# Kernel tuning notes

Hardware: AMD Instinct MI355X
Metric: run time of the kernel (lower is better)

The kernel has to match this reference:

```python
import jax, jax.numpy as jnp
import numpy as np

HID = 1024   # hidden_size
NH = 16      # num_heads
NKV = 4      # num_kv_heads
HD = 64      # head_dim
C = 64       # chunk_size
RATIO = 0.125  # freq_cutoff_ratio
KS = 7       # conv_kernel_size


def setup_inputs() -> dict:
    key = jax.random.key(0)
    ks = jax.random.split(key, 11)
    B, N = 4, 4096
    s = 0.02
    return {
        "hidden_states": jax.random.normal(ks[0], (B, N, HID), jnp.float32),
        "q_w": jax.random.normal(ks[1], (NH * HD, HID), jnp.float32) * s,
        "k_w": jax.random.normal(ks[2], (NKV * HD, HID), jnp.float32) * s,
        "v_w": jax.random.normal(ks[3], (NKV * HD, HID), jnp.float32) * s,
        "o_w": jax.random.normal(ks[4], (HID, NH * HD), jnp.float32) * s,
        "dw_r": jax.random.normal(ks[5], (HID, 1, KS), jnp.float32) * 0.3,
        "pw_r": jax.random.normal(ks[6], (HID, HID), jnp.float32) * s,
        "dw_i": jax.random.normal(ks[7], (HID, 1, KS), jnp.float32) * 0.3,
        "pw_i": jax.random.normal(ks[8], (HID, HID), jnp.float32) * s,
        "gate_w": jax.random.normal(ks[9], (HID, HID), jnp.float32) * s,
        "alpha_raw": jnp.zeros((1,), jnp.float32),
    }


def _block_causal_attention(x, qw, kw, vw, ow, k):
    # x: [B, nc, k, D] real. Flatten chunk freq bins; chunk j attends to chunks 0..j.
    B, nc, _, D = x.shape
    T = nc * k
    xf = x.reshape(B, T, D)
    q = (xf @ qw.T).reshape(B, T, NH, HD).transpose(0, 2, 1, 3)    # [B,H,T,hd]
    kk = (xf @ kw.T).reshape(B, T, NKV, HD).transpose(0, 2, 1, 3)
    v = (xf @ vw.T).reshape(B, T, NKV, HD).transpose(0, 2, 1, 3)
    rep = NH // NKV
    kk = jnp.repeat(kk, rep, axis=1)
    v = jnp.repeat(v, rep, axis=1)
    chunk_ids = jnp.arange(T) // k
    mask = chunk_ids[:, None] >= chunk_ids[None, :]                # [T,T] bool
    scores = jnp.einsum('bhqd,bhkd->bhqk', q, kk) / np.float32(np.sqrt(HD))
    scores = jnp.where(mask[None, None], scores, jnp.finfo(scores.dtype).min)
    p = jax.nn.softmax(scores, axis=-1)
    o = jnp.einsum('bhqk,bhkd->bhqd', p, v)
    o = o.transpose(0, 2, 1, 3).reshape(B, T, NH * HD)
    return (o @ ow.T).reshape(B, nc, k, D)


def _causal_conv(x, dw, pw):
    # x: [B, nc, L, D] real. Depthwise causal conv + GELU + pointwise conv.
    B, nc, L, D = x.shape
    xc = x.reshape(B * nc, L, D).transpose(0, 2, 1)                # [BN, D, L]
    xp = jnp.pad(xc, ((0, 0), (0, 0), (KS - 1, 0)))                # causal left pad
    y = jax.lax.conv_general_dilated(
        xp, dw, window_strides=(1,), padding='VALID',
        dimension_numbers=('NCH', 'OIH', 'NCH'), feature_group_count=D)
    y = jax.nn.gelu(y, approximate=False)
    y = jnp.einsum('ncl,oc->nol', y, pw)                           # 1x1 conv
    return y.transpose(0, 2, 1).reshape(B, nc, L, D)


def _forward(hidden_states, q_w, k_w, v_w, o_w, dw_r, pw_r, dw_i, pw_i, gate_w, alpha_raw):
    B, N, D = hidden_states.shape
    pad_len = (-N) % C
    x = jnp.pad(hidden_states, ((0, 0), (0, pad_len), (0, 0))) if pad_len else hidden_states
    nc = x.shape[1] // C
    chunks = x.reshape(B, nc, C, D)
    Xh = jnp.fft.rfft(chunks.astype(jnp.float32), axis=2)          # [B,nc,M,D] complex
    M = Xh.shape[2]
    k = max(1, int(M * RATIO))
    X_low, X_high = Xh[:, :, :k, :], Xh[:, :, k:, :]
    # low-freq: block-causal attention on real and imag parts separately
    A_r = _block_causal_attention(X_low.real, q_w, k_w, v_w, o_w, k)
    A_i = _block_causal_attention(X_low.imag, q_w, k_w, v_w, o_w, k)
    A_low = jax.lax.complex(A_r, A_i)
    # high-freq: causal conv branch, gated by per-chunk time-domain mean
    H_r = _causal_conv(X_high.real, dw_r, pw_r)
    H_i = _causal_conv(X_high.imag, dw_i, pw_i)
    g = jax.nn.sigmoid(chunks.mean(axis=2) @ gate_w.T)[:, :, None, :]  # [B,nc,1,D]
    A_high = jax.lax.complex(H_r * g, H_i * g) + X_high
    alpha = jax.nn.sigmoid(alpha_raw)                               # [1]
    A_low_fused = alpha * A_low + (1.0 - alpha) * X_low
    Y_hat = jnp.concatenate([A_low_fused, A_high], axis=2)
    Y = jnp.fft.irfft(Y_hat, n=C, axis=2)
    return Y.reshape(B, -1, D)[:, :N, :].astype(hidden_states.dtype)


def reference(hidden_states, q_w, k_w, v_w, o_w, dw_r, pw_r, dw_i, pw_i, gate_w, alpha_raw):
    return _forward(hidden_states, q_w, k_w, v_w, o_w, dw_r, pw_r, dw_i, pw_i, gate_w, alpha_raw)
```

## Files before the change

### kernel.cpp

```cpp
#include <hip/hip_runtime.h>
#include <math.h>


typedef __bf16 bf16_t;
typedef bf16_t bf16x8 __attribute__((ext_vector_type(8)));
typedef float f32x4 __attribute__((ext_vector_type(4)));

#define EP_NONE 0
#define EP_SIGMOID 1
#define EP_FUSELOW 2
#define EP_HIGH 3

__device__ __forceinline__ void gld_lds16(const bf16_t* g, bf16_t* l) {
  __builtin_amdgcn_global_load_lds(
      (const __attribute__((address_space(1))) unsigned int*)g,
      (__attribute__((address_space(3))) unsigned int*)l, 16, 0, 0);
}

__global__ __launch_bounds__(256) void prep_w(
    const float* __restrict__ qw, const float* __restrict__ kw,
    const float* __restrict__ vw, const float* __restrict__ ow,
    const float* __restrict__ gw, const float* __restrict__ pwr,
    const float* __restrict__ pwi, bf16_t* __restrict__ Wqkv,
    bf16_t* __restrict__ owb, bf16_t* __restrict__ gwb,
    bf16_t* __restrict__ pwrb, bf16_t* __restrict__ pwib) {
  int gi = blockIdx.x * 256 + threadIdx.x;
  float4 v;
  bf16_t* o;
  if (gi < 393216) {
    if (gi < 262144) v = ((const float4*)qw)[gi];
    else if (gi < 327680) v = ((const float4*)kw)[gi - 262144];
    else v = ((const float4*)vw)[gi - 327680];
    o = Wqkv + (long)gi * 4;
  } else {
    int j = gi - 393216;
    int sel = j >> 18, off = j & 262143;
    const float* s = sel == 0 ? ow : sel == 1 ? gw : sel == 2 ? pwr : pwi;
    bf16_t* d = sel == 0 ? owb : sel == 1 ? gwb : sel == 2 ? pwrb : pwib;
    v = ((const float4*)s)[off];
    o = d + (long)off * 4;
  }
  o[0] = (bf16_t)v.x; o[1] = (bf16_t)v.y; o[2] = (bf16_t)v.z; o[3] = (bf16_t)v.w;
}

__global__ __launch_bounds__(256) void mk_basis(bf16_t* __restrict__ dhi,
                                                bf16_t* __restrict__ dres,
                                                bf16_t* __restrict__ bhi,
                                                bf16_t* __restrict__ bres,
                                                float* __restrict__ tlow) {
  int idx = blockIdx.x * 256 + threadIdx.x;
  const float TW = 6.283185307179586f / 64.f;
  if (idx < 5120) {
    int r = idx >> 6, k = idx & 63;
    float v = 0.f;
    if (r < 33) {
      v = cosf(TW * (float)((r * k) & 63));
    } else if (r < 66) {
      v = -sinf(TW * (float)(((r - 33) * k) & 63));
    }
    bf16_t h = (bf16_t)v;
    float res = v - (float)h;
    int addr = r * 64 + (((k >> 3) ^ (r & 7)) << 3) + (k & 7);
    dhi[addr] = h;
    dres[addr] = (bf16_t)res;
  } else if (idx < 9216) {
    int i = idx - 5120;
    int t = i >> 6, k = i & 63;
    float v = 0.f;
    if (k < 28) {
      int ft = ((4 + k) * t) & 63;
      v = 2.f * cosf(TW * (float)ft) * (1.f / 64.f);
    } else if (k == 28) {
      int ft = (32 * t) & 63;
      v = cosf(TW * (float)ft) * (1.f / 64.f);
    } else if (k < 57) {
      int ft = ((k - 25) * t) & 63;
      v = -2.f * sinf(TW * (float)ft) * (1.f / 64.f);
    }
    bf16_t h = (bf16_t)v;
    float res = v - (float)h;
    int addr = t * 64 + (((k >> 3) ^ (t & 7)) << 3) + (k & 7);
    bhi[addr] = h;
    bres[addr] = (bf16_t)res;
  } else if (idx < 9728) {
    int i = idx - 9216;
    int t = i >> 3, j = i & 7;
    float v = 0.f;
    if (j == 0) v = 1.f / 64.f;
    else if (j < 7) {
      int f = (j + 1) >> 1;
      int ft = (f * t) & 63;
      float th = TW * (float)ft;
      v = (j & 1) ? 2.f * cosf(th) * (1.f / 64.f)
                  : -2.f * sinf(th) * (1.f / 64.f);
    }
    tlow[i] = v;
  }
}

__global__ __launch_bounds__(128) void dft_mfma(
    const float* __restrict__ X, const bf16_t* __restrict__ dhi,
    const bf16_t* __restrict__ dres, bf16_t* __restrict__ Xh,
    bf16_t* __restrict__ XLr, bf16_t* __restrict__ XLi,
    bf16_t* __restrict__ gmean) {
  const int bc = blockIdx.y;
  const int d0 = blockIdx.x * 128;
  const int tid = threadIdx.x;
  const int lane = tid & 63, wave = tid >> 6;
  const int mr = lane & 15, q = lane >> 4;
  const int wn = wave * 64;

  __shared__ bf16_t Ahi[80 * 64];
  __shared__ bf16_t Ares[80 * 64];
  __shared__ bf16_t Bh[128 * 64];
  __shared__ bf16_t Br[128 * 64];

  for (int i = wave; i < 10; i += 2) {
    gld_lds16(dhi + (i * 64 + lane) * 8, Ahi + i * 512);
    gld_lds16(dres + (i * 64 + lane) * 8, Ares + i * 512);
  }

  {
    const float* xc = X + ((long)bc * 64) * 1024 + d0 + tid;
    const int sw = tid & 7;
#pragma unroll
    for (int g = 0; g < 8; g++) {
      bf16x8 vh, vr;
#pragma unroll
      for (int i = 0; i < 8; i++) {
        float v = xc[(long)(g * 8 + i) * 1024];
        bf16_t h = (bf16_t)v;
        vh[i] = h;
        vr[i] = (bf16_t)(v - (float)h);
      }
      *(bf16x8*)&Bh[tid * 64 + ((g ^ sw) << 3)] = vh;
      *(bf16x8*)&Br[tid * 64 + ((g ^ sw) << 3)] = vr;
    }
  }
  __syncthreads();

  f32x4 acc[5][4];
#pragma unroll
  for (int i = 0; i < 5; i++)
#pragma unroll
    for (int j = 0; j < 4; j++) acc[i][j] = (f32x4){0.f, 0.f, 0.f, 0.f};

#pragma unroll
  for (int s = 0; s < 2; s++) {
    bf16x8 bh[4], br[4];
#pragma unroll
    for (int ni = 0; ni < 4; ni++) {
      int dcol = wn + ni * 16 + mr;
      int so = (((s * 4 + q) ^ (dcol & 7)) << 3);
      bh[ni] = *(const bf16x8*)&Bh[dcol * 64 + so];
      br[ni] = *(const bf16x8*)&Br[dcol * 64 + so];
    }
#pragma unroll
    for (int mi = 0; mi < 5; mi++) {
      int trow = mi * 16 + mr;
      int so = (((s * 4 + q) ^ (trow & 7)) << 3);
      bf16x8 ah = *(const bf16x8*)&Ahi[trow * 64 + so];
      bf16x8 ar = *(const bf16x8*)&Ares[trow * 64 + so];
#pragma unroll
      for (int ni = 0; ni < 4; ni++) {
        acc[mi][ni] = __builtin_amdgcn_mfma_f32_16x16x32_bf16(
            ah, bh[ni], acc[mi][ni], 0, 0, 0);
        acc[mi][ni] = __builtin_amdgcn_mfma_f32_16x16x32_bf16(
            ah, br[ni], acc[mi][ni], 0, 0, 0);
        acc[mi][ni] = __builtin_amdgcn_mfma_f32_16x16x32_bf16(
            ar, bh[ni], acc[mi][ni], 0, 0, 0);
      }
    }
  }

  const int b = bc >> 6, ch = bc & 63;
  bf16_t* xp = Xh + (long)bc * 66 * 1024 + d0;
#pragma unroll
  for (int mi = 0; mi < 5; mi++) {
#pragma unroll
    for (int r = 0; r < 4; r++) {
      int row = mi * 16 + q * 4 + r;
      if (row >= 66) continue;
#pragma unroll
      for (int ni = 0; ni < 4; ni++) {
        int col = wn + ni * 16 + mr;
        float val = acc[mi][ni][r];
        xp[(long)row * 1024 + col] = (bf16_t)val;
        if (row == 0)
          gmean[(long)bc * 1024 + d0 + col] = (bf16_t)(val * (1.f / 64.f));
        if (row < 4)
          XLr[((long)(b * 256 + ch * 4 + row)) * 1024 + d0 + col] = (bf16_t)val;
        if (row >= 33 && row < 37)
          XLi[((long)(b * 256 + ch * 4 + row - 33)) * 1024 + d0 + col] =
              (bf16_t)val;
      }
    }
  }
}

template <int EMODE>
__global__ __launch_bounds__(256, 2) void gemm128(
    const bf16_t* __restrict__ A0, const bf16_t* __restrict__ A1,
    const bf16_t* __restrict__ B0, const bf16_t* __restrict__ B1,
    int N, int ntc, int zc,
    void* __restrict__ C0v, void* __restrict__ C1v,
    const bf16_t* __restrict__ E0, const bf16_t* __restrict__ E1,
    bf16_t* __restrict__ XhMut,
    const float* __restrict__ gate, const float* __restrict__ alpha_ptr) {
  constexpr int K = 1024;
  constexpr int NT = 32;
  __shared__ bf16_t lds[4][2][128 * 32];

  const int nwg = gridDim.x;
  const int g = (blockIdx.x & 7) * (nwg >> 3) + (blockIdx.x >> 3);
  const int per_mt = ntc * zc;
  const int mt = g / per_mt, rem = g - mt * per_mt;
  const int nt = rem % ntc, z = rem / ntc;
  const bf16_t* A = z ? A1 : A0;
  const bf16_t* B = z ? B1 : B0;
  void* Cv = z ? C1v : C0v;
  const bf16_t* E = z ? E1 : E0;
  const int imoff = z ? 33 * 1024 : 0;
  const int m0 = mt * 128, n0 = nt * 128;

  const int tid = threadIdx.x;
  const int lane = tid & 63, wave = tid >> 6;
  const int wm = (wave & 1) * 64, wn = (wave >> 1) * 64;
  const int q = lane >> 4, mr = lane & 15;
  const int srow = tid >> 2, sk8 = (tid & 3) * 8;

  f32x4 acc[4][4];
#pragma unroll
  for (int i = 0; i < 4; i++)
#pragma unroll
    for (int j = 0; j < 4; j++) acc[i][j] = (f32x4){0.f, 0.f, 0.f, 0.f};

  auto stage = [&](int t) {
    const int bi = t & 3;
    const int kb = t * 32;
#pragma unroll
    for (int it = 0; it < 2; it++) {
      gld_lds16(A + (long)(m0 + it * 64 + srow) * K + kb + sk8,
                &lds[bi][0][(it * 256 + wave * 64) * 8]);
      gld_lds16(B + (long)(n0 + it * 64 + srow) * K + kb + sk8,
                &lds[bi][1][(it * 256 + wave * 64) * 8]);
    }
  };

  stage(0);
  stage(1);
  stage(2);

  for (int t = 0; t < NT; t++) {
    if (t < NT - 2)
      asm volatile("s_waitcnt vmcnt(8)" ::: "memory");
    else if (t == NT - 2)
      asm volatile("s_waitcnt vmcnt(4)" ::: "memory");
    else
      asm volatile("s_waitcnt vmcnt(0)" ::: "memory");
    __builtin_amdgcn_sched_barrier(0);
    __builtin_amdgcn_s_barrier();
    if (t + 3 < NT) stage(t + 3);

    const bf16_t* As_ = &lds[t & 3][0][0];
    const bf16_t* Bs_ = &lds[t & 3][1][0];
    bf16x8 bfr[4];
#pragma unroll
    for (int ni = 0; ni < 4; ni++)
      bfr[ni] = *(const bf16x8*)&Bs_[(wn + ni * 16 + mr) * 32 + q * 8];
    __builtin_amdgcn_s_setprio(1);
#pragma unroll
    for (int mi = 0; mi < 4; mi++) {
      bf16x8 af = *(const bf16x8*)&As_[(wm + mi * 16 + mr) * 32 + q * 8];
#pragma unroll
      for (int ni = 0; ni < 4; ni++)
        acc[mi][ni] = __builtin_amdgcn_mfma_f32_16x16x32_bf16(
            af, bfr[ni], acc[mi][ni], 0, 0, 0);
    }
    __builtin_amdgcn_s_setprio(0);
  }

  float alpha = 0.f;
  if constexpr (EMODE == EP_FUSELOW) alpha = 1.f / (1.f + __expf(-alpha_ptr[0]));
#pragma unroll
  for (int mi = 0; mi < 4; mi++) {
#pragma unroll
    for (int ni = 0; ni < 4; ni++) {
      int col = n0 + wn + ni * 16 + mr;
      int rbase = m0 + wm + mi * 16 + q * 4;
#pragma unroll
      for (int r = 0; r < 4; r++) {
        int row = rbase + r;
        float val = acc[mi][ni][r];
        if constexpr (EMODE == EP_NONE) {
          ((bf16_t*)Cv)[(long)row * N + col] = (bf16_t)val;
        } else if constexpr (EMODE == EP_SIGMOID) {
          ((float*)Cv)[(long)row * N + col] = 1.f / (1.f + __expf(-val));
        } else if constexpr (EMODE == EP_FUSELOW) {
          float xl = (float)E[(long)row * 1024 + col];
          ((float*)Cv)[(long)row * 1024 + col] = alpha * val + (1.f - alpha) * xl;
        } else {
          int bc = row / 29, l = row - bc * 29;
          long x = ((long)bc * 66 + 4 + l) * 1024 + imoff + col;
          XhMut[x] = (bf16_t)fmaf(val, gate[(long)bc * 1024 + col], (float)XhMut[x]);
        }
      }
    }
  }
}

__global__ __launch_bounds__(256) void attn_mfma(const bf16_t* __restrict__ QKVr,
                                                 const bf16_t* __restrict__ QKVi,
                                                 bf16_t* __restrict__ Or_,
                                                 bf16_t* __restrict__ Oi_) {
  const int h = blockIdx.x;
  const int b = blockIdx.y >> 2, qt = blockIdx.y & 3;
  const bf16_t* QKV = blockIdx.z ? QKVi : QKVr;
  bf16_t* O = blockIdx.z ? Oi_ : Or_;
  const int kvh = h >> 2;
  const int tid = threadIdx.x;
  const int lane = tid & 63, wave = tid >> 6;
  const int mr = lane & 15, q4 = lane >> 4;

  __shared__ bf16_t Ks[64 * 72];
  __shared__ bf16_t Vt[64 * 72];
  __shared__ bf16_t Ps[4][16 * 72];

  bf16x8 af[2];
  {
    const bf16_t* qp =
        QKV + (long)(b * 256 + qt * 64 + wave * 16 + mr) * 1536 + h * 64;
    af[0] = *(const bf16x8*)(qp + q4 * 8);
    af[1] = *(const bf16x8*)(qp + 32 + q4 * 8);
  }
  f32x4 Oacc[4];
#pragma unroll
  for (int ni = 0; ni < 4; ni++) Oacc[ni] = (f32x4){0.f, 0.f, 0.f, 0.f};
  float mrow[4], lrow[4];
#pragma unroll
  for (int r = 0; r < 4; r++) { mrow[r] = -1e30f; lrow[r] = 0.f; }

  for (int kt = 0; kt <= qt; kt++) {
#pragma unroll
    for (int it = 0; it < 2; it++) {
      int idx = tid + it * 256;
      int key = idx >> 3, dg = idx & 7;
      const bf16_t* kp = QKV + (long)(b * 256 + kt * 64 + key) * 1536 + 1024 +
                         kvh * 64 + dg * 8;
      *(bf16x8*)&Ks[key * 72 + dg * 8] = *(const bf16x8*)kp;
      bf16x8 vv = *(const bf16x8*)(kp + 256);
#pragma unroll
      for (int j = 0; j < 8; j++) Vt[(dg * 8 + j) * 72 + key] = vv[j];
    }
    __syncthreads();

    f32x4 S[4];
#pragma unroll
    for (int ni = 0; ni < 4; ni++) {
      S[ni] = (f32x4){0.f, 0.f, 0.f, 0.f};
#pragma unroll
      for (int s = 0; s < 2; s++) {
        bf16x8 kb = *(const bf16x8*)&Ks[(ni * 16 + mr) * 72 + s * 32 + q4 * 8];
        S[ni] = __builtin_amdgcn_mfma_f32_16x16x32_bf16(af[s], kb, S[ni], 0, 0, 0);
      }
    }
#pragma unroll
    for (int ni = 0; ni < 4; ni++) {
#pragma unroll
      for (int r = 0; r < 4; r++) {
        float v = S[ni][r] * 0.125f;
        if (kt == qt) {
          int qrow = wave * 16 + q4 * 4 + r;
          int kcol = ni * 16 + mr;
          if ((qrow >> 2) < (kcol >> 2)) v = -1e30f;
        }
        S[ni][r] = v;
      }
    }
#pragma unroll
    for (int r = 0; r < 4; r++) {
      float mx = fmaxf(fmaxf(S[0][r], S[1][r]), fmaxf(S[2][r], S[3][r]));
#pragma unroll
      for (int off = 1; off < 16; off <<= 1) mx = fmaxf(mx, __shfl_xor(mx, off));
      float mn = fmaxf(mrow[r], mx);
      float sc = __expf(mrow[r] - mn);
      mrow[r] = mn;
      float rs = 0.f;
#pragma unroll
      for (int ni = 0; ni < 4; ni++) {
        float p = __expf(S[ni][r] - mn);
        rs += p;
        Ps[wave][(q4 * 4 + r) * 72 + ni * 16 + mr] = (bf16_t)p;
      }
#pragma unroll
      for (int off = 1; off < 16; off <<= 1) rs += __shfl_xor(rs, off);
      lrow[r] = lrow[r] * sc + rs;
#pragma unroll
      for (int ni = 0; ni < 4; ni++) Oacc[ni][r] *= sc;
    }
    bf16x8 pa[2];
    pa[0] = *(const bf16x8*)&Ps[wave][mr * 72 + q4 * 8];
    pa[1] = *(const bf16x8*)&Ps[wave][mr * 72 + 32 + q4 * 8];
#pragma unroll
    for (int ni = 0; ni < 4; ni++) {
#pragma unroll
      for (int s = 0; s < 2; s++) {
        bf16x8 vb = *(const bf16x8*)&Vt[(ni * 16 + mr) * 72 + s * 32 + q4 * 8];
        Oacc[ni] = __builtin_amdgcn_mfma_f32_16x16x32_bf16(pa[s], vb, Oacc[ni], 0, 0, 0);
      }
    }
    __syncthreads();
  }

#pragma unroll
  for (int r = 0; r < 4; r++) {
    float inv = 1.f / lrow[r];
    long row = b * 256 + qt * 64 + wave * 16 + q4 * 4 + r;
#pragma unroll
    for (int ni = 0; ni < 4; ni++)
      O[row * 1024 + h * 64 + ni * 16 + mr] = (bf16_t)(Oacc[ni][r] * inv);
  }
}

__global__ __launch_bounds__(256) void dwconv_kernel(const bf16_t* __restrict__ Xh,
                                                     const float* __restrict__ dwr,
                                                     const float* __restrict__ dwi,
                                                     bf16_t* __restrict__ Gr,
                                                     bf16_t* __restrict__ Gi) {
  const int d = blockIdx.x * 256 + threadIdx.x;
  const int bc = blockIdx.y;
  const float* dw = blockIdx.z ? dwi : dwr;
  bf16_t* G = blockIdx.z ? Gi : Gr;
  const int imoff = blockIdx.z ? 33 * 1024 : 0;
  float w[7];
#pragma unroll
  for (int j = 0; j < 7; j++) w[j] = dw[d * 7 + j];
  float x[29];
#pragma unroll
  for (int l = 0; l < 29; l++)
    x[l] = (float)Xh[((long)bc * 66 + 4 + l) * 1024 + imoff + d];
#pragma unroll
  for (int l = 0; l < 29; l++) {
    float y = 0.f;
#pragma unroll
    for (int j = 0; j < 7; j++) {
      int src = l - 6 + j;
      if (src >= 0) y = fmaf(w[j], x[src], y);
    }
    float ge = 0.5f * y * (1.f + erff(y * 0.7071067811865475f));
    G[((long)bc * 29 + l) * 1024 + d] = (bf16_t)ge;
  }
}

__global__ __launch_bounds__(128) void irfft_mfma(
    const bf16_t* __restrict__ Xh, const float* __restrict__ Afr,
    const float* __restrict__ Afi, const bf16_t* __restrict__ bhi,
    const bf16_t* __restrict__ bres, const float* __restrict__ tlow,
    float* __restrict__ out) {
  const int bc = blockIdx.y;
  const int d0 = blockIdx.x * 128;
  const int tid = threadIdx.x;
  const int lane = tid & 63, wave = tid >> 6;
  const int mr = lane & 15, q = lane >> 4;
  const int wn = wave * 64;

  __shared__ bf16_t Ahi[64 * 64];
  __shared__ bf16_t Ares[64 * 64];
  __shared__ bf16_t Bs[128 * 64];
  __shared__ float Tl[64 * 8];

  for (int i = wave; i < 8; i += 2) {
    gld_lds16(bhi + (i * 64 + lane) * 8, Ahi + i * 512);
    gld_lds16(bres + (i * 64 + lane) * 8, Ares + i * 512);
  }
  ((float4*)Tl)[tid] = ((const float4*)tlow)[tid];

  {
    const bf16_t* xc = Xh + (long)bc * 66 * 1024 + d0 + tid;
    const int sw = tid & 7;
#pragma unroll
    for (int g = 0; g < 8; g++) {
      bf16x8 v;
#pragma unroll
      for (int i = 0; i < 8; i++) {
        int j = g * 8 + i;
        int row = (j < 29) ? (4 + j) : (8 + j);
        v[i] = (j < 57) ? xc[(long)row * 1024] : (bf16_t)0.f;
      }
      *(bf16x8*)&Bs[tid * 64 + ((g ^ sw) << 3)] = v;
    }
  }
  __syncthreads();

  f32x4 acc[4][4];
#pragma unroll
  for (int i = 0; i < 4; i++)
#pragma unroll
    for (int j = 0; j < 4; j++) acc[i][j] = (f32x4){0.f, 0.f, 0.f, 0.f};

#pragma unroll
  for (int s = 0; s < 2; s++) {
    bf16x8 bfv[4];
#pragma unroll
    for (int ni = 0; ni < 4; ni++) {
      int dcol = wn + ni * 16 + mr;
      bfv[ni] = *(const bf16x8*)&Bs[dcol * 64 + (((s * 4 + q) ^ (dcol & 7)) << 3)];
    }
#pragma unroll
    for (int mi = 0; mi < 4; mi++) {
      int trow = mi * 16 + mr;
      int so = (((s * 4 + q) ^ (trow & 7)) << 3);
      bf16x8 ah = *(const bf16x8*)&Ahi[trow * 64 + so];
      bf16x8 ar = *(const bf16x8*)&Ares[trow * 64 + so];
#pragma unroll
      for (int ni = 0; ni < 4; ni++) {
        acc[mi][ni] = __builtin_amdgcn_mfma_f32_16x16x32_bf16(
            ah, bfv[ni], acc[mi][ni], 0, 0, 0);
        acc[mi][ni] = __builtin_amdgcn_mfma_f32_16x16x32_bf16(
            ar, bfv[ni], acc[mi][ni], 0, 0, 0);
      }
    }
  }

  const int arow = (bc >> 6) * 256 + (bc & 63) * 4;
  float R[4][7];
#pragma unroll
  for (int ni = 0; ni < 4; ni++) {
    long ab = (long)arow * 1024 + d0 + wn + ni * 16 + mr;
    R[ni][0] = Afr[ab];
    R[ni][1] = Afr[ab + 1024];
    R[ni][2] = Afi[ab + 1024];
    R[ni][3] = Afr[ab + 2048];
    R[ni][4] = Afi[ab + 2048];
    R[ni][5] = Afr[ab + 3072];
    R[ni][6] = Afi[ab + 3072];
  }
  const long obase = ((long)bc * 64) * 1024 + d0;
#pragma unroll
  for (int mi = 0; mi < 4; mi++) {
#pragma unroll
    for (int r = 0; r < 4; r++) {
      int t = mi * 16 + q * 4 + r;
      const float* tl = &Tl[t * 8];
#pragma unroll
      for (int ni = 0; ni < 4; ni++) {
        float low = tl[0] * R[ni][0];
        low = fmaf(tl[1], R[ni][1], low);
        low = fmaf(tl[2], R[ni][2], low);
        low = fmaf(tl[3], R[ni][3], low);
        low = fmaf(tl[4], R[ni][4], low);
        low = fmaf(tl[5], R[ni][5], low);
        low = fmaf(tl[6], R[ni][6], low);
        out[obase + (long)t * 1024 + wn + ni * 16 + mr] = acc[mi][ni][r] + low;
      }
    }
  }
}

extern "C" void kernel_launch(void* const* d_in, const int* in_sizes, int n_in,
                              void* d_out, int out_size, void* d_ws, size_t ws_size,
                              hipStream_t stream) {
  const float* hidden = (const float*)d_in[0];
  const float* q_w = (const float*)d_in[1];
  const float* k_w = (const float*)d_in[2];
  const float* v_w = (const float*)d_in[3];
  const float* o_w = (const float*)d_in[4];
  const float* dw_r = (const float*)d_in[5];
  const float* pw_r = (const float*)d_in[6];
  const float* dw_i = (const float*)d_in[7];
  const float* pw_i = (const float*)d_in[8];
  const float* gate_w = (const float*)d_in[9];
  const float* alpha_raw = (const float*)d_in[10];
  float* out = (float*)d_out;

  float* ws = (float*)d_ws;
  float* Afr = ws;
  float* Afi = Afr + 1048576;
  float* gg = Afi + 1048576;
  bf16_t* bws = (bf16_t*)(gg + 262144);
  bf16_t* Xh = bws;
  bf16_t* Wqkv_b = Xh + 17301504;
  bf16_t* ow_b = Wqkv_b + 1572864;
  bf16_t* gw_b = ow_b + 1048576;
  bf16_t* pwr_b = gw_b + 1048576;
  bf16_t* pwi_b = pwr_b + 1048576;
  bf16_t* XLr = pwi_b + 1048576;
  bf16_t* XLi = XLr + 1048576;
  bf16_t* gmean = XLi + 1048576;
  bf16_t* QKVbr = gmean + 262144;
  bf16_t* QKVbi = QKVbr + 1572864;
  bf16_t* Obr = QKVbi + 1572864;
  bf16_t* Obi = Obr + 1048576;
  bf16_t* Gr = Obi + 1048576;
  bf16_t* Gi = Gr + 7602176;
  bf16_t* bhi = Gi + 7602176;
  bf16_t* bres = bhi + 4096;
  bf16_t* dbhi = bres + 4096;
  bf16_t* dbres = dbhi + 5120;
  float* tlowp = (float*)(dbres + 5120);

  mk_basis<<<38, 256, 0, stream>>>(dbhi, dbres, bhi, bres, tlowp);
  dft_mfma<<<dim3(8, 256), 128, 0, stream>>>(hidden, dbhi, dbres, Xh, XLr,
                                             XLi, gmean);
  prep_w<<<5632, 256, 0, stream>>>(q_w, k_w, v_w, o_w, gate_w, pw_r, pw_i,
                                   Wqkv_b, ow_b, gw_b, pwr_b, pwi_b);
  gemm128<EP_NONE><<<192, 256, 0, stream>>>(
      XLr, XLi, Wqkv_b, Wqkv_b, 1536, 12, 2, QKVbr, QKVbi, nullptr, nullptr,
      nullptr, nullptr, nullptr);
  gemm128<EP_SIGMOID><<<16, 256, 0, stream>>>(
      gmean, gmean, gw_b, gw_b, 1024, 8, 1, gg, gg, nullptr, nullptr,
      nullptr, nullptr, nullptr);
  attn_mfma<<<dim3(16, 16, 2), 256, 0, stream>>>(QKVbr, QKVbi, Obr, Obi);
  gemm128<EP_FUSELOW><<<128, 256, 0, stream>>>(
      Obr, Obi, ow_b, ow_b, 1024, 8, 2, Afr, Afi, XLr, XLi,
      nullptr, nullptr, alpha_raw);
  dwconv_kernel<<<dim3(4, 256, 2), 256, 0, stream>>>(Xh, dw_r, dw_i, Gr, Gi);
  gemm128<EP_HIGH><<<928, 256, 0, stream>>>(
      Gr, Gi, pwr_b, pwi_b, 1024, 8, 2, nullptr, nullptr, nullptr, nullptr,
      Xh, gg, nullptr);
  irfft_mfma<<<dim3(8, 256), 128, 0, stream>>>(Xh, Afr, Afi, bhi, bres,
                                               tlowp, out);
}
```

Baseline: 317.8 us.

## Use 256x256-tile GEMM for high-freq pointwise conv; read DFT bases from global

The high-frequency pointwise-conv GEMM moves from a 128x128-tile kernel with 928 blocks to a dedicated 256x256-tile kernel with 512 threads, 232 blocks, a 4-stage LDS pipeline using global_load_lds and a new XOR swizzle. The larger tile is meant to raise data reuse and cut LDS and global traffic per MFMA, at the cost of more registers per thread and fewer blocks for load balancing. Separately, the DFT and irfft kernels stop staging the basis matrices in LDS and read them directly from global memory (now stored unswizzled), which frees shared memory and drops a load-and-sync step but relies on cache hits for repeated reads.

```diff
diff --git a/kernel.cpp b/kernel.cpp
--- a/kernel.cpp
+++ b/kernel.cpp
@@ -60,9 +60,8 @@
     }
     bf16_t h = (bf16_t)v;
     float res = v - (float)h;
-    int addr = r * 64 + (((k >> 3) ^ (r & 7)) << 3) + (k & 7);
-    dhi[addr] = h;
-    dres[addr] = (bf16_t)res;
+    dhi[idx] = h;
+    dres[idx] = (bf16_t)res;
   } else if (idx < 9216) {
     int i = idx - 5120;
     int t = i >> 6, k = i & 63;
@@ -79,9 +78,8 @@
     }
     bf16_t h = (bf16_t)v;
     float res = v - (float)h;
-    int addr = t * 64 + (((k >> 3) ^ (t & 7)) << 3) + (k & 7);
-    bhi[addr] = h;
-    bres[addr] = (bf16_t)res;
+    bhi[i] = h;
+    bres[i] = (bf16_t)res;
   } else if (idx < 9728) {
     int i = idx - 9216;
     int t = i >> 3, j = i & 7;
@@ -110,15 +108,8 @@
   const int mr = lane & 15, q = lane >> 4;
   const int wn = wave * 64;
 
-  __shared__ bf16_t Ahi[80 * 64];
-  __shared__ bf16_t Ares[80 * 64];
   __shared__ bf16_t Bh[128 * 64];
   __shared__ bf16_t Br[128 * 64];
-
-  for (int i = wave; i < 10; i += 2) {
-    gld_lds16(dhi + (i * 64 + lane) * 8, Ahi + i * 512);
-    gld_lds16(dres + (i * 64 + lane) * 8, Ares + i * 512);
-  }
 
   {
     const float* xc = X + ((long)bc * 64) * 1024 + d0 + tid;
@@ -158,9 +149,8 @@
 #pragma unroll
     for (int mi = 0; mi < 5; mi++) {
       int trow = mi * 16 + mr;
-      int so = (((s * 4 + q) ^ (trow & 7)) << 3);
-      bf16x8 ah = *(const bf16x8*)&Ahi[trow * 64 + so];
-      bf16x8 ar = *(const bf16x8*)&Ares[trow * 64 + so];
+      bf16x8 ah = *(const bf16x8*)&dhi[trow * 64 + (s * 4 + q) * 8];
+      bf16x8 ar = *(const bf16x8*)&dres[trow * 64 + (s * 4 + q) * 8];
 #pragma unroll
       for (int ni = 0; ni < 4; ni++) {
         acc[mi][ni] = __builtin_amdgcn_mfma_f32_16x16x32_bf16(
@@ -205,8 +195,7 @@
     int N, int ntc, int zc,
     void* __restrict__ C0v, void* __restrict__ C1v,
     const bf16_t* __restrict__ E0, const bf16_t* __restrict__ E1,
-    bf16_t* __restrict__ XhMut,
-    const float* __restrict__ gate, const float* __restrict__ alpha_ptr) {
+    const float* __restrict__ alpha_ptr) {
   constexpr int K = 1024;
   constexpr int NT = 32;
   __shared__ bf16_t lds[4][2][128 * 32];
@@ -220,7 +209,6 @@
   const bf16_t* B = z ? B1 : B0;
   void* Cv = z ? C1v : C0v;
   const bf16_t* E = z ? E1 : E0;
-  const int imoff = z ? 33 * 1024 : 0;
   const int m0 = mt * 128, n0 = nt * 128;
 
   const int tid = threadIdx.x;
@@ -296,14 +284,105 @@
           ((bf16_t*)Cv)[(long)row * N + col] = (bf16_t)val;
         } else if constexpr (EMODE == EP_SIGMOID) {
           ((float*)Cv)[(long)row * N + col] = 1.f / (1.f + __expf(-val));
-        } else if constexpr (EMODE == EP_FUSELOW) {
+        } else {
           float xl = (float)E[(long)row * 1024 + col];
           ((float*)Cv)[(long)row * 1024 + col] = alpha * val + (1.f - alpha) * xl;
-        } else {
-          int bc = row / 29, l = row - bc * 29;
-          long x = ((long)bc * 66 + 4 + l) * 1024 + imoff + col;
-          XhMut[x] = (bf16_t)fmaf(val, gate[(long)bc * 1024 + col], (float)XhMut[x]);
         }
+      }
+    }
+  }
+}
+
+__global__ __launch_bounds__(512, 2) void gemm256_high(
+    const bf16_t* __restrict__ A0, const bf16_t* __restrict__ A1,
+    const bf16_t* __restrict__ B0, const bf16_t* __restrict__ B1,
+    bf16_t* __restrict__ XhMut, const float* __restrict__ gate) {
+  constexpr int K = 1024;
+  constexpr int NT = K / 32;
+  __shared__ bf16_t lds[4][2][256 * 32];
+
+  const int id = blockIdx.x;
+  const int kk = (id & 7) * 29 + (id >> 3);
+  const int mt = kk >> 3, rem = kk & 7;
+  const int nt = rem & 3, z = rem >> 2;
+  const bf16_t* A = z ? A1 : A0;
+  const bf16_t* B = z ? B1 : B0;
+  const int imoff = z ? 33 * 1024 : 0;
+  const int m0 = mt * 256, n0 = nt * 256;
+
+  const int tid = threadIdx.x;
+  const int lane = tid & 63, wave = tid >> 6;
+  const int wm = (wave & 1) * 128, wn = (wave >> 1) * 64;
+  const int q = lane >> 4, mr = lane & 15;
+  const int srow = tid >> 2;
+  const int gk8 = (((tid & 3) ^ ((((tid >> 2) & 3) + ((tid >> 4) & 3)) & 3)) << 3);
+
+  f32x4 acc[8][4];
+#pragma unroll
+  for (int i = 0; i < 8; i++)
+#pragma unroll
+    for (int j = 0; j < 4; j++) acc[i][j] = (f32x4){0.f, 0.f, 0.f, 0.f};
+
+  auto stage = [&](int t) {
+    const int bi = t & 3;
+    const int kb = t * 32;
+#pragma unroll
+    for (int rd = 0; rd < 2; rd++) {
+      gld_lds16(A + (long)(m0 + rd * 128 + srow) * K + kb + gk8,
+                &lds[bi][0][(rd * 512 + wave * 64) * 8]);
+      gld_lds16(B + (long)(n0 + rd * 128 + srow) * K + kb + gk8,
+                &lds[bi][1][(rd * 512 + wave * 64) * 8]);
+    }
+  };
+
+  stage(0);
+  stage(1);
+  stage(2);
+
+  const int asl = (q ^ (((mr & 3) + ((mr >> 2) & 3)) & 3)) * 8;
+
+  for (int t = 0; t < NT; t++) {
+    if (t < NT - 2)
+      asm volatile("s_waitcnt vmcnt(8)" ::: "memory");
+    else if (t == NT - 2)
+      asm volatile("s_waitcnt vmcnt(4)" ::: "memory");
+    else
+      asm volatile("s_waitcnt vmcnt(0)" ::: "memory");
+    __builtin_amdgcn_sched_barrier(0);
+    __builtin_amdgcn_s_barrier();
+    if (t + 3 < NT) stage(t + 3);
+
+    const bf16_t* As_ = &lds[t & 3][0][0];
+    const bf16_t* Bs_ = &lds[t & 3][1][0];
+    bf16x8 bfr[4];
+#pragma unroll
+    for (int ni = 0; ni < 4; ni++)
+      bfr[ni] = *(const bf16x8*)&Bs_[(wn + ni * 16 + mr) * 32 + asl];
+    __builtin_amdgcn_s_setprio(1);
+#pragma unroll
+    for (int mi = 0; mi < 8; mi++) {
+      bf16x8 af = *(const bf16x8*)&As_[(wm + mi * 16 + mr) * 32 + asl];
+#pragma unroll
+      for (int ni = 0; ni < 4; ni++)
+        acc[mi][ni] = __builtin_amdgcn_mfma_f32_16x16x32_bf16(
+            af, bfr[ni], acc[mi][ni], 0, 0, 0);
+    }
+    __builtin_amdgcn_s_setprio(0);
+  }
+
+#pragma unroll
+  for (int mi = 0; mi < 8; mi++) {
+#pragma unroll
+    for (int r = 0; r < 4; r++) {
+      int row = m0 + wm + mi * 16 + q * 4 + r;
+      int bc = row / 29, l = row - bc * 29;
+      long xbase = ((long)bc * 66 + 4 + l) * 1024 + imoff;
+      const float* gp = gate + (long)bc * 1024;
+#pragma unroll
+      for (int ni = 0; ni < 4; ni++) {
+        int col = n0 + wn + ni * 16 + mr;
+        long x = xbase + col;
+        XhMut[x] = (bf16_t)fmaf(acc[mi][ni][r], gp[col], (float)XhMut[x]);
       }
     }
   }
@@ -464,15 +543,9 @@
   const int mr = lane & 15, q = lane >> 4;
   const int wn = wave * 64;
 
-  __shared__ bf16_t Ahi[64 * 64];
-  __shared__ bf16_t Ares[64 * 64];
   __shared__ bf16_t Bs[128 * 64];
   __shared__ float Tl[64 * 8];
 
-  for (int i = wave; i < 8; i += 2) {
-    gld_lds16(bhi + (i * 64 + lane) * 8, Ahi + i * 512);
-    gld_lds16(bres + (i * 64 + lane) * 8, Ares + i * 512);
-  }
   ((float4*)Tl)[tid] = ((const float4*)tlow)[tid];
 
   {
@@ -509,9 +582,8 @@
 #pragma unroll
     for (int mi = 0; mi < 4; mi++) {
       int trow = mi * 16 + mr;
-      int so = (((s * 4 + q) ^ (trow & 7)) << 3);
-      bf16x8 ah = *(const bf16x8*)&Ahi[trow * 64 + so];
-      bf16x8 ar = *(const bf16x8*)&Ares[trow * 64 + so];
+      bf16x8 ah = *(const bf16x8*)&bhi[trow * 64 + (s * 4 + q) * 8];
+      bf16x8 ar = *(const bf16x8*)&bres[trow * 64 + (s * 4 + q) * 8];
 #pragma unroll
       for (int ni = 0; ni < 4; ni++) {
         acc[mi][ni] = __builtin_amdgcn_mfma_f32_16x16x32_bf16(
@@ -606,18 +678,15 @@
                                    Wqkv_b, ow_b, gw_b, pwr_b, pwi_b);
   gemm128<EP_NONE><<<192, 256, 0, stream>>>(
       XLr, XLi, Wqkv_b, Wqkv_b, 1536, 12, 2, QKVbr, QKVbi, nullptr, nullptr,
-      nullptr, nullptr, nullptr);
+      nullptr);
   gemm128<EP_SIGMOID><<<16, 256, 0, stream>>>(
       gmean, gmean, gw_b, gw_b, 1024, 8, 1, gg, gg, nullptr, nullptr,
-      nullptr, nullptr, nullptr);
+      nullptr);
   attn_mfma<<<dim3(16, 16, 2), 256, 0, stream>>>(QKVbr, QKVbi, Obr, Obi);
   gemm128<EP_FUSELOW><<<128, 256, 0, stream>>>(
-      Obr, Obi, ow_b, ow_b, 1024, 8, 2, Afr, Afi, XLr, XLi,
-      nullptr, nullptr, alpha_raw);
+      Obr, Obi, ow_b, ow_b, 1024, 8, 2, Afr, Afi, XLr, XLi, alpha_raw);
   dwconv_kernel<<<dim3(4, 256, 2), 256, 0, stream>>>(Xh, dw_r, dw_i, Gr, Gi);
-  gemm128<EP_HIGH><<<928, 256, 0, stream>>>(
-      Gr, Gi, pwr_b, pwi_b, 1024, 8, 2, nullptr, nullptr, nullptr, nullptr,
-      Xh, gg, nullptr);
+  gemm256_high<<<dim3(232), 512, 0, stream>>>(Gr, Gi, pwr_b, pwi_b, Xh, gg);
   irfft_mfma<<<dim3(8, 256), 128, 0, stream>>>(Xh, Afr, Afi, bhi, bres,
                                                tlowp, out);
 }
```

After: 324.2 us. 2.0% more time.
